# Kernel optimization log

Measured on AMD Instinct MI355X. Metric: run time of the kernel, lower is better.

Reference implementation:

```python
import jax, jax.numpy as jnp
import numpy as np

N = 16384          # number of proposals (batch dim already squeezed)
FEAT = 512         # CLIP ViT-B/32 embedding dim
NUM_CATS = 65      # background + 64 categories
K = 25             # max_boxes_to_return
NMS_THRESH = 0.6
MAX_DETS = 1000    # nms() default max_dets
MIN_RPN_SCORE = 0.9
MIN_BOX_AREA = 220.0


def setup_inputs() -> dict:
    key = jax.random.key(0)
    ks = jax.random.split(key, 9)
    # valid (ymin, xmin, ymax, xmax) boxes in a ~1000px image
    y1 = jax.random.uniform(ks[0], (N,)) * 900.0
    x1 = jax.random.uniform(ks[1], (N,)) * 900.0
    h = 40.0 + jax.random.uniform(ks[2], (N,)) * 160.0
    w = 40.0 + jax.random.uniform(ks[3], (N,)) * 160.0
    detection_boxes = jnp.stack([y1, x1, y1 + h, x1 + w], axis=-1)
    roi_boxes = jax.random.uniform(ks[4], (N, 4))
    roi_scores = jax.random.uniform(ks[5], (N,))
    visual_features = jax.random.normal(ks[6], (N, FEAT))
    visual_features = visual_features / jnp.linalg.norm(visual_features, axis=-1, keepdims=True)
    text_features = jax.random.normal(ks[7], (NUM_CATS, FEAT))
    text_features = text_features / jnp.linalg.norm(text_features, axis=-1, keepdims=True)
    detection_masks = jax.random.uniform(ks[8], (N, 33, 33))
    # row 2 of image_info holds (y_scale, x_scale)
    image_info = jnp.ones((5, 2), jnp.float32).at[2].set(jnp.array([0.8, 0.8], jnp.float32))
    return {
        'roi_boxes': roi_boxes,
        'roi_scores': roi_scores,
        'detection_boxes': detection_boxes,
        'detection_masks': detection_masks,
        'visual_features': visual_features,
        'image_info': image_info,
        'text_features': text_features,
    }


def greedy_nms_keep(boxes, scores, thresh, max_dets):
    """Greedy IoU NMS; returns boolean keep mask over original indices."""
    n = boxes.shape[0]
    order = jnp.argsort(-scores)           # descending by score
    b = boxes[order]
    y1, x1, y2, x2 = b[:, 0], b[:, 1], b[:, 2], b[:, 3]
    areas = (x2 - x1) * (y2 - y1)
    pos = jnp.arange(n)

    def body(i, state):
        suppressed, keep, cnt = state
        valid = jnp.logical_and(~suppressed[i], cnt < max_dets)
        iw = jnp.maximum(0.0, jnp.minimum(x2[i], x2) - jnp.maximum(x1[i], x1))
        ih = jnp.maximum(0.0, jnp.minimum(y2[i], y2) - jnp.maximum(y1[i], y1))
        inter = iw * ih
        iou = inter / (areas[i] + areas - inter + 1e-12)
        suppressed = suppressed | (valid & (iou > thresh) & (pos > i))
        keep = keep.at[i].set(valid)
        return suppressed, keep, cnt + valid.astype(jnp.int32)

    init = (jnp.zeros(n, bool), jnp.zeros(n, bool), jnp.int32(0))
    _, keep_sorted, _ = jax.lax.fori_loop(0, n, body, init)
    return jnp.zeros(n, bool).at[order].set(keep_sorted)


def reference(roi_boxes, roi_scores, detection_boxes, detection_masks,
              visual_features, image_info, text_features):
    image_scale = jnp.tile(image_info[2:3, :], (1, 2))          # [1,4]
    rescaled = detection_boxes / image_scale                     # [N,4]
    keep = greedy_nms_keep(detection_boxes, roi_scores, NMS_THRESH, MAX_DETS)
    box_sizes = (rescaled[:, 2] - rescaled[:, 0]) * (rescaled[:, 3] - rescaled[:, 1])
    valid = (keep
             & ~jnp.all(roi_boxes == 0.0, axis=-1)
             & (roi_scores >= MIN_RPN_SCORE)
             & (box_sizes > MIN_BOX_AREA))
    # first K valid indices in original order (fixed-shape compaction)
    idx = jnp.nonzero(valid, size=K, fill_value=0)[0]
    row_valid = jnp.arange(K) < jnp.minimum(valid.sum(), K)
    det_feat = visual_features[idx]                              # [K,512]
    det_resc = rescaled[idx]                                     # [K,4]
    scores_all = det_feat @ text_features.T                      # [K,C]; use_softmax=False
    max_s = jnp.max(scores_all, axis=1)
    fg = row_valid & (jnp.argmax(scores_all, axis=1) != 0)       # drop background argmax
    sort_key = jnp.where(fg, max_s, -jnp.inf)
    order = jnp.argsort(-sort_key)                               # fg rows first, by max score
    mask = fg[order]
    ymin, xmin, ymax, xmax = det_resc[:, 0], det_resc[:, 1], det_resc[:, 2], det_resc[:, 3]
    processed = jnp.stack([xmin, ymin, xmax, ymax], axis=-1)     # [K,4] xyxy
    bboxes = jnp.where(mask[:, None], processed[order], 0.0)
    scores = jnp.where(mask[:, None], scores_all[order][:, 1:], 0.0)  # drop bg column
    return scores, bboxes, mask
```

## Files before the change

kernel.cpp:

```cpp
#include <hip/hip_runtime.h>
#include <math.h>

#define N 16384
#define NWORDS 256
#define FEAT 512
#define NUM_CATS 65
#define K 25
#define MAX_DETS 1000


__global__ void k_build(const float* __restrict__ scores,
                        unsigned long long* __restrict__ ckeys,
                        unsigned int* __restrict__ rank,
                        int* __restrict__ ticket) {
    int i = blockIdx.x * 256 + threadIdx.x;
    float s = scores[i];
    rank[i] = 0u;
    bool cand = s >= 0.9f;
    unsigned long long bal = __ballot(cand);
    int lane = threadIdx.x & 63;
    int base = 0;
    if (lane == 0) base = atomicAdd(ticket, (int)__popcll(bal));
    base = __shfl(base, 0, 64);
    if (cand) {
        int pre = (int)__popcll(bal & ((1ull << lane) - 1ull));
        ckeys[base + pre] =
            ((unsigned long long)__float_as_uint(s) << 32) |
            (unsigned long long)(0xFFFFFFFFu - (unsigned)i);
    }
}

__global__ void k_crank(const unsigned long long* __restrict__ ckeys,
                        const int* __restrict__ ticket,
                        const float* __restrict__ det_boxes,
                        unsigned int* __restrict__ rank,
                        float4* __restrict__ sbox,
                        float* __restrict__ sarea) {
    int nc = *ticket;
    if (nc < 0) nc = 0;
    if (nc > N) nc = N;
    if (blockIdx.x * 256 >= nc) return;
    __shared__ unsigned long long lk[2048];
    int ci = blockIdx.x * 256 + threadIdx.x;
    unsigned long long my = (ci < nc) ? ckeys[ci] : 0ull;
    unsigned int cnt = 0;
    for (int j0 = 0; j0 < nc; j0 += 2048) {
        int m = nc - j0; if (m > 2048) m = 2048;
        __syncthreads();
        for (int t2 = threadIdx.x; t2 < m; t2 += 256) lk[t2] = ckeys[j0 + t2];
        __syncthreads();
        if (ci < nc) {
#pragma unroll 8
            for (int t2 = 0; t2 < m; ++t2) cnt += (lk[t2] > my) ? 1u : 0u;
        }
    }
    if (ci < nc) {
        unsigned int o = 0xFFFFFFFFu - (unsigned int)my;
        rank[o] = cnt;
        float4 b = ((const float4*)det_boxes)[o];
        sbox[cnt] = b;
        sarea[cnt] = (b.w - b.y) * (b.z - b.x);
    }
}

__global__ void k_mask(const float4* __restrict__ sbox,
                       const float* __restrict__ sarea,
                       const int* __restrict__ ticket,
                       unsigned long long* __restrict__ mask) {
    int ncand = *ticket;
    if (ncand < 0) ncand = 0;
    if (ncand > N) ncand = N;
    int NC = (ncand + 63) >> 6;
    int total = NC * (NC + 1) / 2;
    __shared__ float4 cbox[64];
    __shared__ float carea[64];
    int t = threadIdx.x;
    for (int tile = blockIdx.x; tile < total; tile += gridDim.x) {
        int cb = (int)((sqrtf(8.0f * (float)tile + 1.0f) - 1.0f) * 0.5f);
        while ((cb + 1) * (cb + 2) / 2 <= tile) ++cb;
        while (cb * (cb + 1) / 2 > tile) --cb;
        int rb = tile - cb * (cb + 1) / 2;

        __syncthreads();
        int col0 = cb * 64;
        cbox[t] = sbox[col0 + t];
        carea[t] = sarea[col0 + t];
        __syncthreads();
        int row = rb * 64 + t;
        float4 r = sbox[row];
        float ra = sarea[row];
        unsigned long long bits = 0ull;
        for (int j = 0; j < 64; ++j) {
            int col = col0 + j;
            if (col > row) {
                float4 cbx = cbox[j];
                float iw = fminf(r.w, cbx.w) - fmaxf(r.y, cbx.y);
                iw = fmaxf(iw, 0.0f);
                float ih = fminf(r.z, cbx.z) - fmaxf(r.x, cbx.x);
                ih = fmaxf(ih, 0.0f);
                float inter = iw * ih;
                float iou = inter / (ra + carea[j] - inter + 1e-12f);
                if (iou > 0.6f) bits |= (1ull << j);
            }
        }
        mask[(size_t)row * NWORDS + cb] = bits;
    }
}

__global__ void __launch_bounds__(64, 1)
k_scan(const unsigned long long* __restrict__ mask,
       const int* __restrict__ ticket,
       unsigned long long* __restrict__ keepw_ws) {
    __shared__ unsigned long long keepw_arr[NWORDS];
    __shared__ int keptList[1024];
    int lane = threadIdx.x;
    for (int i2 = lane; i2 < NWORDS; i2 += 64) keepw_arr[i2] = 0ull;

    int ncand = *ticket;
    if (ncand < 0) ncand = 0;
    if (ncand > N) ncand = N;
    int NC = (ncand + 63) >> 6;

    int cnt = 0, nk = 0;
    unsigned long long dnext = 0ull;
    if (NC > 0) dnext = mask[(size_t)lane * NWORDS];

    for (int c = 0; c < NC; ++c) {
        if (cnt >= MAX_DETS) break;

        unsigned long long dcur = dnext;
        if (c + 1 < NC)
            dnext = mask[(size_t)((c + 1) * 64 + lane) * NWORDS + (c + 1)];
        unsigned int dlo = (unsigned int)dcur;
        unsigned int dhi = (unsigned int)(dcur >> 32);

        unsigned long long acc = 0ull;
        {
            int q = lane;
            while (q < nk) {
#define GS(i)                                                             \
                unsigned long long G##i = 0ull;                           \
                {                                                         \
                    int qq = q + 64 * i;                                  \
                    if (qq < nk) {                                        \
                        int t = keptList[qq];                             \
                        G##i = mask[(size_t)t * NWORDS + c];              \
                    }                                                     \
                }
                GS(0) GS(1) GS(2) GS(3) GS(4) GS(5) GS(6) GS(7)
#undef GS
                acc |= G0 | G1 | G2 | G3 | G4 | G5 | G6 | G7;
                q += 512;
            }
        }
        unsigned int alo = (unsigned int)acc;
        unsigned int ahi = (unsigned int)(acc >> 32);
        for (int off = 32; off > 0; off >>= 1) {
            alo |= (unsigned int)__shfl_xor((int)alo, off, 64);
            ahi |= (unsigned int)__shfl_xor((int)ahi, off, 64);
        }
        unsigned long long sw =
            ((unsigned long long)(unsigned int)__builtin_amdgcn_readfirstlane(
                 (int)ahi) << 32) |
             (unsigned long long)(unsigned int)__builtin_amdgcn_readfirstlane(
                 (int)alo);
        unsigned long long alive = ~sw;
        if (ncand - c * 64 < 64)
            alive &= ((1ull << (ncand - c * 64)) - 1ull);

        unsigned long long zb = __ballot(dcur == 0ull);

        unsigned long long keepw = 0ull;
        unsigned long long NZ = alive & ~zb;
        while (true) {
            unsigned long long below;
            int t = -1;
            if (NZ) { t = __ffsll((long long)NZ) - 1; below = (1ull << t) - 1ull; }
            else below = ~0ull;
            unsigned long long seg = alive & below;
            int segc = (int)__popcll(seg);
            if (cnt + segc >= MAX_DETS) {
                int allow = MAX_DETS - cnt;
                unsigned long long r = 0ull;
                for (int k2 = 0; k2 < allow; ++k2) {
                    unsigned long long b = seg & (~seg + 1ull);
                    r |= b; seg ^= b;
                }
                keepw |= r; cnt = MAX_DETS; break;
            }
            keepw |= seg; cnt += segc; alive &= ~seg;
            if (t < 0) break;
            keepw |= (1ull << t); ++cnt;
            if (cnt >= MAX_DETS) break;
            unsigned long long dt =
                ((unsigned long long)(unsigned int)__builtin_amdgcn_readlane(
                     (int)dhi, t) << 32) |
                 (unsigned long long)(unsigned int)__builtin_amdgcn_readlane(
                     (int)dlo, t);
            alive &= ~(dt | (1ull << t));
            NZ &= alive;
            NZ &= ~(1ull << t);
        }
        if (lane == 0) keepw_arr[c] = keepw;

        if (keepw != 0ull) {
            if ((keepw >> lane) & 1ull) {
                int pre = (int)__popcll(keepw & ((1ull << lane) - 1ull));
                keptList[nk + pre] = c * 64 + lane;
            }
            nk += (int)__popcll(keepw);
        }
    }

    for (int i2 = lane; i2 < NWORDS; i2 += 64) keepw_ws[i2] = keepw_arr[i2];
}

__global__ void k_valid(const unsigned long long* __restrict__ keepw_ws,
                        const unsigned int* __restrict__ rank,
                        const float* __restrict__ roi_boxes,
                        const float* __restrict__ roi_scores,
                        const float* __restrict__ det_boxes,
                        const float* __restrict__ info,
                        unsigned long long* __restrict__ validw) {
    int i = blockIdx.x * 256 + threadIdx.x;
    float sy = info[4], sx = info[5];
    unsigned int r = rank[i];
    bool keep = ((keepw_ws[(r >> 6) & (NWORDS - 1)] >> (r & 63)) & 1ull) != 0ull;
    float4 rb = ((const float4*)roi_boxes)[i];
    bool nz = !((rb.x == 0.0f) && (rb.y == 0.0f) && (rb.z == 0.0f) && (rb.w == 0.0f));
    bool sc = roi_scores[i] >= 0.9f;
    float4 db = ((const float4*)det_boxes)[i];
    float r0 = db.x / sy, r1 = db.y / sx, r2 = db.z / sy, r3 = db.w / sx;
    bool big = ((r2 - r0) * (r3 - r1)) > 220.0f;
    bool valid = keep && nz && sc && big;
    unsigned long long bal = __ballot(valid);
    if ((threadIdx.x & 63) == 0) validw[i >> 6] = bal;
}

__device__ __forceinline__ void pick_first_k(
        const unsigned long long* __restrict__ validw,
        int* idxL, int* cntL, int tid) {
    if (tid < K) idxL[tid] = 0;
    __syncthreads();
    if (tid < 64) {
        int lane = tid;
        unsigned long long w0 = validw[lane * 4 + 0];
        unsigned long long w1 = validw[lane * 4 + 1];
        unsigned long long w2 = validw[lane * 4 + 2];
        unsigned long long w3 = validw[lane * 4 + 3];
        int s = (int)(__popcll(w0) + __popcll(w1) + __popcll(w2) + __popcll(w3));
        int pref = s;
        for (int off = 1; off < 64; off <<= 1) {
            int v = __shfl_up(pref, off, 64);
            if (lane >= off) pref += v;
        }
        int excl = pref - s;
        int total = __shfl(pref, 63, 64);
        if (lane == 0) *cntL = total;
        if (excl < K) {
            unsigned long long wsv[4] = { w0, w1, w2, w3 };
            int rk = excl;
            for (int q = 0; q < 4; ++q) {
                unsigned long long ww = wsv[q];
                while (ww && rk < K) {
                    int j = __ffsll((long long)ww) - 1;
                    ww &= ww - 1ull;
                    idxL[rk++] = (lane * 4 + q) * 64 + j;
                }
            }
        }
    }
    __syncthreads();
}

__global__ void k_gemm(const unsigned long long* __restrict__ validw,
                       const float* __restrict__ vis,
                       const float* __restrict__ tf,
                       float* __restrict__ scoresW) {
    __shared__ int idxL[K];
    __shared__ int cntL;
    __shared__ float featL[FEAT];
    int tid = threadIdx.x;
    pick_first_k(validw, idxL, &cntL, tid);
    int o = idxL[blockIdx.x];
    if (tid < 128)
        ((float4*)featL)[tid] = ((const float4*)(vis + (size_t)o * FEAT))[tid];
    __syncthreads();
    if (tid < NUM_CATS) {
        const float* tr = &tf[(size_t)tid * FEAT];
        float s = 0.0f;
#pragma unroll 8
        for (int e = 0; e < FEAT; ++e) s += featL[e] * tr[e];
        scoresW[blockIdx.x * NUM_CATS + tid] = s;
    }
}

__global__ void k_final(const unsigned long long* __restrict__ validw,
                        const float* __restrict__ scoresW,
                        const float* __restrict__ det_boxes,
                        const float* __restrict__ info,
                        float* __restrict__ out) {
    __shared__ int idxL[K];
    __shared__ int cntL;
    __shared__ float scL[K * NUM_CATS];
    __shared__ float keyL[K];
    __shared__ int fgL[K];
    __shared__ int ordL[K];
    int tid = threadIdx.x;
    pick_first_k(validw, idxL, &cntL, tid);

    for (int p = tid; p < K * NUM_CATS; p += 256) scL[p] = scoresW[p];
    __syncthreads();

    int count = cntL;
    int mincount = count < K ? count : K;

    if (tid < K) {
        float mv = scL[tid * NUM_CATS];
        int ma = 0;
        for (int c = 1; c < NUM_CATS; ++c) {
            float v = scL[tid * NUM_CATS + c];
            if (v > mv) { mv = v; ma = c; }
        }
        int fg = (tid < mincount) && (ma != 0);
        fgL[tid] = fg;
        keyL[tid] = fg ? mv : -INFINITY;
    }
    __syncthreads();

    if (tid == 0) {
        unsigned used = 0;
        for (int p = 0; p < K; ++p) {
            int bk = -1; float bv = 0.0f;
            for (int k2 = 0; k2 < K; ++k2) {
                if (used & (1u << k2)) continue;
                if (bk < 0 || keyL[k2] > bv) { bk = k2; bv = keyL[k2]; }
            }
            ordL[p] = bk;
            used |= (1u << bk);
        }
    }
    __syncthreads();

    float sy = info[4], sx = info[5];
    for (int p = tid; p < K * (NUM_CATS - 1); p += 256) {
        int q = p >> 6, cc = p & 63;
        int src = ordL[q];
        out[p] = fgL[src] ? scL[src * NUM_CATS + cc + 1] : 0.0f;
    }
    for (int p = tid; p < K * 4; p += 256) {
        int q = p >> 2, e = p & 3;
        int src = ordL[q];
        float v = 0.0f;
        if (fgL[src]) {
            int o = idxL[src];
            float b0 = det_boxes[o * 4 + 0] / sy;
            float b1 = det_boxes[o * 4 + 1] / sx;
            float b2 = det_boxes[o * 4 + 2] / sy;
            float b3 = det_boxes[o * 4 + 3] / sx;
            v = (e == 0) ? b1 : (e == 1) ? b0 : (e == 2) ? b3 : b2;
        }
        out[1600 + p] = v;
    }
    if (tid < K) out[1700 + tid] = fgL[ordL[tid]] ? 1.0f : 0.0f;
}

extern "C" void kernel_launch(void* const* d_in, const int* in_sizes, int n_in,
                              void* d_out, int out_size, void* d_ws, size_t ws_size,
                              hipStream_t stream) {
    const float* roi_boxes  = (const float*)d_in[0];
    const float* roi_scores = (const float*)d_in[1];
    const float* det_boxes  = (const float*)d_in[2];
    const float* vis        = (const float*)d_in[4];
    const float* info       = (const float*)d_in[5];
    const float* tf         = (const float*)d_in[6];

    char* ws = (char*)d_ws;
    unsigned long long* ckeys = (unsigned long long*)(ws + 0);
    unsigned int* rank        = (unsigned int*)(ws + 131072);
    float4* sbox              = (float4*)(ws + 262144);
    float* sarea              = (float*)(ws + 524288);
    unsigned long long* mask  = (unsigned long long*)(ws + 589824);
    int* idxArr               = (int*)(ws + 34144256);
    unsigned long long* keepw = (unsigned long long*)(ws + 34144384);
    unsigned long long* validw= (unsigned long long*)(ws + 34146432);
    float* scoresW            = (float*)(ws + 34148480);
    int* ticket               = idxArr + 30;

    hipMemsetAsync(idxArr, 0, 128, stream);
    k_build<<<64, 256, 0, stream>>>(roi_scores, ckeys, rank, ticket);
    k_crank<<<64, 256, 0, stream>>>(ckeys, ticket, det_boxes, rank, sbox, sarea);
    k_mask<<<1024, 64, 0, stream>>>(sbox, sarea, ticket, mask);
    k_scan<<<1, 64, 0, stream>>>(mask, ticket, keepw);
    k_valid<<<64, 256, 0, stream>>>(keepw, rank, roi_boxes, roi_scores,
                                    det_boxes, info, validw);
    k_gemm<<<K, 256, 0, stream>>>(validw, vis, tf, scoresW);
    k_final<<<1, 256, 0, stream>>>(validw, scoresW, det_boxes, info, (float*)d_out);
}
```

Baseline: 231.7 us.

## Fuse all pipeline stages into one cooperative kernel with grid syncs

Replaces the memset and seven separate kernel launches with a single cooperative kernel of 64 blocks that separates the stages with grid-wide syncs. The IoU mask stage now gives each wavefront its own tile and broadcasts column boxes with shuffles instead of LDS. This removes per-launch overhead and inter-kernel gaps. In exchange, the mask stage runs on only 64 blocks instead of 1024, and each grid.sync adds its own cost.

```diff
diff --git a/kernel.cpp b/kernel.cpp
--- a/kernel.cpp
+++ b/kernel.cpp
@@ -1,5 +1,8 @@
 #include <hip/hip_runtime.h>
+#include <hip/hip_cooperative_groups.h>
 #include <math.h>
+
+namespace cg = cooperative_groups;
 
 #define N 16384
 #define NWORDS 256
@@ -8,234 +11,6 @@
 #define K 25
 #define MAX_DETS 1000
 
-
-__global__ void k_build(const float* __restrict__ scores,
-                        unsigned long long* __restrict__ ckeys,
-                        unsigned int* __restrict__ rank,
-                        int* __restrict__ ticket) {
-    int i = blockIdx.x * 256 + threadIdx.x;
-    float s = scores[i];
-    rank[i] = 0u;
-    bool cand = s >= 0.9f;
-    unsigned long long bal = __ballot(cand);
-    int lane = threadIdx.x & 63;
-    int base = 0;
-    if (lane == 0) base = atomicAdd(ticket, (int)__popcll(bal));
-    base = __shfl(base, 0, 64);
-    if (cand) {
-        int pre = (int)__popcll(bal & ((1ull << lane) - 1ull));
-        ckeys[base + pre] =
-            ((unsigned long long)__float_as_uint(s) << 32) |
-            (unsigned long long)(0xFFFFFFFFu - (unsigned)i);
-    }
-}
-
-__global__ void k_crank(const unsigned long long* __restrict__ ckeys,
-                        const int* __restrict__ ticket,
-                        const float* __restrict__ det_boxes,
-                        unsigned int* __restrict__ rank,
-                        float4* __restrict__ sbox,
-                        float* __restrict__ sarea) {
-    int nc = *ticket;
-    if (nc < 0) nc = 0;
-    if (nc > N) nc = N;
-    if (blockIdx.x * 256 >= nc) return;
-    __shared__ unsigned long long lk[2048];
-    int ci = blockIdx.x * 256 + threadIdx.x;
-    unsigned long long my = (ci < nc) ? ckeys[ci] : 0ull;
-    unsigned int cnt = 0;
-    for (int j0 = 0; j0 < nc; j0 += 2048) {
-        int m = nc - j0; if (m > 2048) m = 2048;
-        __syncthreads();
-        for (int t2 = threadIdx.x; t2 < m; t2 += 256) lk[t2] = ckeys[j0 + t2];
-        __syncthreads();
-        if (ci < nc) {
-#pragma unroll 8
-            for (int t2 = 0; t2 < m; ++t2) cnt += (lk[t2] > my) ? 1u : 0u;
-        }
-    }
-    if (ci < nc) {
-        unsigned int o = 0xFFFFFFFFu - (unsigned int)my;
-        rank[o] = cnt;
-        float4 b = ((const float4*)det_boxes)[o];
-        sbox[cnt] = b;
-        sarea[cnt] = (b.w - b.y) * (b.z - b.x);
-    }
-}
-
-__global__ void k_mask(const float4* __restrict__ sbox,
-                       const float* __restrict__ sarea,
-                       const int* __restrict__ ticket,
-                       unsigned long long* __restrict__ mask) {
-    int ncand = *ticket;
-    if (ncand < 0) ncand = 0;
-    if (ncand > N) ncand = N;
-    int NC = (ncand + 63) >> 6;
-    int total = NC * (NC + 1) / 2;
-    __shared__ float4 cbox[64];
-    __shared__ float carea[64];
-    int t = threadIdx.x;
-    for (int tile = blockIdx.x; tile < total; tile += gridDim.x) {
-        int cb = (int)((sqrtf(8.0f * (float)tile + 1.0f) - 1.0f) * 0.5f);
-        while ((cb + 1) * (cb + 2) / 2 <= tile) ++cb;
-        while (cb * (cb + 1) / 2 > tile) --cb;
-        int rb = tile - cb * (cb + 1) / 2;
-
-        __syncthreads();
-        int col0 = cb * 64;
-        cbox[t] = sbox[col0 + t];
-        carea[t] = sarea[col0 + t];
-        __syncthreads();
-        int row = rb * 64 + t;
-        float4 r = sbox[row];
-        float ra = sarea[row];
-        unsigned long long bits = 0ull;
-        for (int j = 0; j < 64; ++j) {
-            int col = col0 + j;
-            if (col > row) {
-                float4 cbx = cbox[j];
-                float iw = fminf(r.w, cbx.w) - fmaxf(r.y, cbx.y);
-                iw = fmaxf(iw, 0.0f);
-                float ih = fminf(r.z, cbx.z) - fmaxf(r.x, cbx.x);
-                ih = fmaxf(ih, 0.0f);
-                float inter = iw * ih;
-                float iou = inter / (ra + carea[j] - inter + 1e-12f);
-                if (iou > 0.6f) bits |= (1ull << j);
-            }
-        }
-        mask[(size_t)row * NWORDS + cb] = bits;
-    }
-}
-
-__global__ void __launch_bounds__(64, 1)
-k_scan(const unsigned long long* __restrict__ mask,
-       const int* __restrict__ ticket,
-       unsigned long long* __restrict__ keepw_ws) {
-    __shared__ unsigned long long keepw_arr[NWORDS];
-    __shared__ int keptList[1024];
-    int lane = threadIdx.x;
-    for (int i2 = lane; i2 < NWORDS; i2 += 64) keepw_arr[i2] = 0ull;
-
-    int ncand = *ticket;
-    if (ncand < 0) ncand = 0;
-    if (ncand > N) ncand = N;
-    int NC = (ncand + 63) >> 6;
-
-    int cnt = 0, nk = 0;
-    unsigned long long dnext = 0ull;
-    if (NC > 0) dnext = mask[(size_t)lane * NWORDS];
-
-    for (int c = 0; c < NC; ++c) {
-        if (cnt >= MAX_DETS) break;
-
-        unsigned long long dcur = dnext;
-        if (c + 1 < NC)
-            dnext = mask[(size_t)((c + 1) * 64 + lane) * NWORDS + (c + 1)];
-        unsigned int dlo = (unsigned int)dcur;
-        unsigned int dhi = (unsigned int)(dcur >> 32);
-
-        unsigned long long acc = 0ull;
-        {
-            int q = lane;
-            while (q < nk) {
-#define GS(i)                                                             \
-                unsigned long long G##i = 0ull;                           \
-                {                                                         \
-                    int qq = q + 64 * i;                                  \
-                    if (qq < nk) {                                        \
-                        int t = keptList[qq];                             \
-                        G##i = mask[(size_t)t * NWORDS + c];              \
-                    }                                                     \
-                }
-                GS(0) GS(1) GS(2) GS(3) GS(4) GS(5) GS(6) GS(7)
-#undef GS
-                acc |= G0 | G1 | G2 | G3 | G4 | G5 | G6 | G7;
-                q += 512;
-            }
-        }
-        unsigned int alo = (unsigned int)acc;
-        unsigned int ahi = (unsigned int)(acc >> 32);
-        for (int off = 32; off > 0; off >>= 1) {
-            alo |= (unsigned int)__shfl_xor((int)alo, off, 64);
-            ahi |= (unsigned int)__shfl_xor((int)ahi, off, 64);
-        }
-        unsigned long long sw =
-            ((unsigned long long)(unsigned int)__builtin_amdgcn_readfirstlane(
-                 (int)ahi) << 32) |
-             (unsigned long long)(unsigned int)__builtin_amdgcn_readfirstlane(
-                 (int)alo);
-        unsigned long long alive = ~sw;
-        if (ncand - c * 64 < 64)
-            alive &= ((1ull << (ncand - c * 64)) - 1ull);
-
-        unsigned long long zb = __ballot(dcur == 0ull);
-
-        unsigned long long keepw = 0ull;
-        unsigned long long NZ = alive & ~zb;
-        while (true) {
-            unsigned long long below;
-            int t = -1;
-            if (NZ) { t = __ffsll((long long)NZ) - 1; below = (1ull << t) - 1ull; }
-            else below = ~0ull;
-            unsigned long long seg = alive & below;
-            int segc = (int)__popcll(seg);
-            if (cnt + segc >= MAX_DETS) {
-                int allow = MAX_DETS - cnt;
-                unsigned long long r = 0ull;
-                for (int k2 = 0; k2 < allow; ++k2) {
-                    unsigned long long b = seg & (~seg + 1ull);
-                    r |= b; seg ^= b;
-                }
-                keepw |= r; cnt = MAX_DETS; break;
-            }
-            keepw |= seg; cnt += segc; alive &= ~seg;
-            if (t < 0) break;
-            keepw |= (1ull << t); ++cnt;
-            if (cnt >= MAX_DETS) break;
-            unsigned long long dt =
-                ((unsigned long long)(unsigned int)__builtin_amdgcn_readlane(
-                     (int)dhi, t) << 32) |
-                 (unsigned long long)(unsigned int)__builtin_amdgcn_readlane(
-                     (int)dlo, t);
-            alive &= ~(dt | (1ull << t));
-            NZ &= alive;
-            NZ &= ~(1ull << t);
-        }
-        if (lane == 0) keepw_arr[c] = keepw;
-
-        if (keepw != 0ull) {
-            if ((keepw >> lane) & 1ull) {
-                int pre = (int)__popcll(keepw & ((1ull << lane) - 1ull));
-                keptList[nk + pre] = c * 64 + lane;
-            }
-            nk += (int)__popcll(keepw);
-        }
-    }
-
-    for (int i2 = lane; i2 < NWORDS; i2 += 64) keepw_ws[i2] = keepw_arr[i2];
-}
-
-__global__ void k_valid(const unsigned long long* __restrict__ keepw_ws,
-                        const unsigned int* __restrict__ rank,
-                        const float* __restrict__ roi_boxes,
-                        const float* __restrict__ roi_scores,
-                        const float* __restrict__ det_boxes,
-                        const float* __restrict__ info,
-                        unsigned long long* __restrict__ validw) {
-    int i = blockIdx.x * 256 + threadIdx.x;
-    float sy = info[4], sx = info[5];
-    unsigned int r = rank[i];
-    bool keep = ((keepw_ws[(r >> 6) & (NWORDS - 1)] >> (r & 63)) & 1ull) != 0ull;
-    float4 rb = ((const float4*)roi_boxes)[i];
-    bool nz = !((rb.x == 0.0f) && (rb.y == 0.0f) && (rb.z == 0.0f) && (rb.w == 0.0f));
-    bool sc = roi_scores[i] >= 0.9f;
-    float4 db = ((const float4*)det_boxes)[i];
-    float r0 = db.x / sy, r1 = db.y / sx, r2 = db.z / sy, r3 = db.w / sx;
-    bool big = ((r2 - r0) * (r3 - r1)) > 220.0f;
-    bool valid = keep && nz && sc && big;
-    unsigned long long bal = __ballot(valid);
-    if ((threadIdx.x & 63) == 0) validw[i >> 6] = bal;
-}
 
 __device__ __forceinline__ void pick_first_k(
         const unsigned long long* __restrict__ validw,
@@ -273,96 +48,312 @@
     __syncthreads();
 }
 
-__global__ void k_gemm(const unsigned long long* __restrict__ validw,
-                       const float* __restrict__ vis,
-                       const float* __restrict__ tf,
-                       float* __restrict__ scoresW) {
-    __shared__ int idxL[K];
-    __shared__ int cntL;
+__global__ void __launch_bounds__(256, 1)
+k_all(const float* __restrict__ roi_boxes,
+      const float* __restrict__ roi_scores,
+      const float* __restrict__ det_boxes,
+      const float* __restrict__ vis,
+      const float* __restrict__ info,
+      const float* __restrict__ tf,
+      unsigned long long* __restrict__ ckeys,
+      unsigned int* __restrict__ rank,
+      float4* __restrict__ sbox,
+      float* __restrict__ sarea,
+      unsigned long long* __restrict__ mask,
+      int* __restrict__ ticket,
+      unsigned long long* __restrict__ keepw_ws,
+      unsigned long long* __restrict__ validw,
+      float* __restrict__ scoresW,
+      float* __restrict__ out) {
+    cg::grid_group grid = cg::this_grid();
+    int bid = blockIdx.x, tid = threadIdx.x;
+    int gi = bid * 256 + tid;
+    int lane = tid & 63;
+    int wv = tid >> 6;
+
+    __shared__ unsigned long long lk[2048];
+    __shared__ unsigned long long keepw_arr[NWORDS];
+    __shared__ int keptList[1024];
     __shared__ float featL[FEAT];
-    int tid = threadIdx.x;
-    pick_first_k(validw, idxL, &cntL, tid);
-    int o = idxL[blockIdx.x];
-    if (tid < 128)
-        ((float4*)featL)[tid] = ((const float4*)(vis + (size_t)o * FEAT))[tid];
-    __syncthreads();
-    if (tid < NUM_CATS) {
-        const float* tr = &tf[(size_t)tid * FEAT];
-        float s = 0.0f;
-#pragma unroll 8
-        for (int e = 0; e < FEAT; ++e) s += featL[e] * tr[e];
-        scoresW[blockIdx.x * NUM_CATS + tid] = s;
-    }
-}
-
-__global__ void k_final(const unsigned long long* __restrict__ validw,
-                        const float* __restrict__ scoresW,
-                        const float* __restrict__ det_boxes,
-                        const float* __restrict__ info,
-                        float* __restrict__ out) {
-    __shared__ int idxL[K];
-    __shared__ int cntL;
     __shared__ float scL[K * NUM_CATS];
     __shared__ float keyL[K];
     __shared__ int fgL[K];
     __shared__ int ordL[K];
-    int tid = threadIdx.x;
-    pick_first_k(validw, idxL, &cntL, tid);
-
-    for (int p = tid; p < K * NUM_CATS; p += 256) scL[p] = scoresW[p];
-    __syncthreads();
-
-    int count = cntL;
-    int mincount = count < K ? count : K;
-
-    if (tid < K) {
-        float mv = scL[tid * NUM_CATS];
-        int ma = 0;
-        for (int c = 1; c < NUM_CATS; ++c) {
-            float v = scL[tid * NUM_CATS + c];
-            if (v > mv) { mv = v; ma = c; }
-        }
-        int fg = (tid < mincount) && (ma != 0);
-        fgL[tid] = fg;
-        keyL[tid] = fg ? mv : -INFINITY;
-    }
-    __syncthreads();
-
-    if (tid == 0) {
-        unsigned used = 0;
-        for (int p = 0; p < K; ++p) {
-            int bk = -1; float bv = 0.0f;
-            for (int k2 = 0; k2 < K; ++k2) {
-                if (used & (1u << k2)) continue;
-                if (bk < 0 || keyL[k2] > bv) { bk = k2; bv = keyL[k2]; }
-            }
-            ordL[p] = bk;
-            used |= (1u << bk);
-        }
-    }
-    __syncthreads();
-
-    float sy = info[4], sx = info[5];
-    for (int p = tid; p < K * (NUM_CATS - 1); p += 256) {
-        int q = p >> 6, cc = p & 63;
-        int src = ordL[q];
-        out[p] = fgL[src] ? scL[src * NUM_CATS + cc + 1] : 0.0f;
-    }
-    for (int p = tid; p < K * 4; p += 256) {
-        int q = p >> 2, e = p & 3;
-        int src = ordL[q];
-        float v = 0.0f;
-        if (fgL[src]) {
-            int o = idxL[src];
-            float b0 = det_boxes[o * 4 + 0] / sy;
-            float b1 = det_boxes[o * 4 + 1] / sx;
-            float b2 = det_boxes[o * 4 + 2] / sy;
-            float b3 = det_boxes[o * 4 + 3] / sx;
-            v = (e == 0) ? b1 : (e == 1) ? b0 : (e == 2) ? b3 : b2;
-        }
-        out[1600 + p] = v;
-    }
-    if (tid < K) out[1700 + tid] = fgL[ordL[tid]] ? 1.0f : 0.0f;
+    __shared__ int idxL[K];
+    __shared__ int cntL;
+
+    if (gi == 0) *ticket = 0;
+    grid.sync();
+
+    {
+        float s = roi_scores[gi];
+        rank[gi] = 0u;
+        bool cand = s >= 0.9f;
+        unsigned long long bal = __ballot(cand);
+        int base = 0;
+        if (lane == 0) base = atomicAdd(ticket, (int)__popcll(bal));
+        base = __shfl(base, 0, 64);
+        if (cand) {
+            int pre = (int)__popcll(bal & ((1ull << lane) - 1ull));
+            ckeys[base + pre] =
+                ((unsigned long long)__float_as_uint(s) << 32) |
+                (unsigned long long)(0xFFFFFFFFu - (unsigned)gi);
+        }
+    }
+    grid.sync();
+
+    int nc = *ticket;
+    if (nc < 0) nc = 0;
+    if (nc > N) nc = N;
+    int NC = (nc + 63) >> 6;
+
+    if (bid * 256 < nc) {
+        int ci = gi;
+        unsigned long long my = (ci < nc) ? ckeys[ci] : 0ull;
+        unsigned int cnt = 0;
+        for (int j0 = 0; j0 < nc; j0 += 2048) {
+            int m = nc - j0; if (m > 2048) m = 2048;
+            __syncthreads();
+            for (int t2 = tid; t2 < m; t2 += 256) lk[t2] = ckeys[j0 + t2];
+            __syncthreads();
+            if (ci < nc) {
+#pragma unroll 8
+                for (int t2 = 0; t2 < m; ++t2) cnt += (lk[t2] > my) ? 1u : 0u;
+            }
+        }
+        if (ci < nc) {
+            unsigned int o = 0xFFFFFFFFu - (unsigned int)my;
+            rank[o] = cnt;
+            float4 b = ((const float4*)det_boxes)[o];
+            sbox[cnt] = b;
+            sarea[cnt] = (b.w - b.y) * (b.z - b.x);
+        }
+    }
+    grid.sync();
+
+    {
+        int total = NC * (NC + 1) / 2;
+        for (int tile = bid * 4 + wv; tile < total; tile += 256) {
+            int cb = (int)((sqrtf(8.0f * (float)tile + 1.0f) - 1.0f) * 0.5f);
+            while ((cb + 1) * (cb + 2) / 2 <= tile) ++cb;
+            while (cb * (cb + 1) / 2 > tile) --cb;
+            int rb = tile - cb * (cb + 1) / 2;
+            int col0 = cb * 64;
+            float4 cbm = sbox[col0 + lane];
+            float cam = sarea[col0 + lane];
+            int row = rb * 64 + lane;
+            float4 r = sbox[row];
+            float ra = sarea[row];
+            unsigned long long bits = 0ull;
+            for (int j = 0; j < 64; ++j) {
+                float bx = __shfl(cbm.x, j, 64);
+                float by = __shfl(cbm.y, j, 64);
+                float bz = __shfl(cbm.z, j, 64);
+                float bw = __shfl(cbm.w, j, 64);
+                float ba = __shfl(cam, j, 64);
+                int col = col0 + j;
+                if (col > row) {
+                    float iw = fminf(r.w, bw) - fmaxf(r.y, by);
+                    iw = fmaxf(iw, 0.0f);
+                    float ih = fminf(r.z, bz) - fmaxf(r.x, bx);
+                    ih = fmaxf(ih, 0.0f);
+                    float inter = iw * ih;
+                    float iou = inter / (ra + ba - inter + 1e-12f);
+                    if (iou > 0.6f) bits |= (1ull << j);
+                }
+            }
+            mask[(size_t)row * NWORDS + cb] = bits;
+        }
+    }
+    grid.sync();
+
+    if (bid == 0 && tid < 64) {
+        for (int i2 = lane; i2 < NWORDS; i2 += 64) keepw_arr[i2] = 0ull;
+
+        int cnt = 0, nk = 0;
+        unsigned long long dnext = 0ull;
+        if (NC > 0) dnext = mask[(size_t)lane * NWORDS];
+
+        for (int c = 0; c < NC; ++c) {
+            if (cnt >= MAX_DETS) break;
+
+            unsigned long long dcur = dnext;
+            if (c + 1 < NC)
+                dnext = mask[(size_t)((c + 1) * 64 + lane) * NWORDS + (c + 1)];
+            unsigned int dlo = (unsigned int)dcur;
+            unsigned int dhi = (unsigned int)(dcur >> 32);
+
+            unsigned long long acc = 0ull;
+            {
+                int q = lane;
+                while (q < nk) {
+#define GS(i)                                                             \
+                    unsigned long long G##i = 0ull;                       \
+                    {                                                     \
+                        int qq = q + 64 * i;                              \
+                        if (qq < nk) {                                    \
+                            int t = keptList[qq];                         \
+                            G##i = mask[(size_t)t * NWORDS + c];          \
+                        }                                                 \
+                    }
+                    GS(0) GS(1) GS(2) GS(3) GS(4) GS(5) GS(6) GS(7)
+#undef GS
+                    acc |= G0 | G1 | G2 | G3 | G4 | G5 | G6 | G7;
+                    q += 512;
+                }
+            }
+            unsigned int alo = (unsigned int)acc;
+            unsigned int ahi = (unsigned int)(acc >> 32);
+            for (int off = 32; off > 0; off >>= 1) {
+                alo |= (unsigned int)__shfl_xor((int)alo, off, 64);
+                ahi |= (unsigned int)__shfl_xor((int)ahi, off, 64);
+            }
+            unsigned long long sw =
+                ((unsigned long long)(unsigned int)__builtin_amdgcn_readfirstlane(
+                     (int)ahi) << 32) |
+                 (unsigned long long)(unsigned int)__builtin_amdgcn_readfirstlane(
+                     (int)alo);
+            unsigned long long alive = ~sw;
+            if (nc - c * 64 < 64)
+                alive &= ((1ull << (nc - c * 64)) - 1ull);
+
+            unsigned long long zb = __ballot(dcur == 0ull);
+
+            unsigned long long keepw = 0ull;
+            unsigned long long NZ = alive & ~zb;
+            while (true) {
+                unsigned long long below;
+                int t = -1;
+                if (NZ) { t = __ffsll((long long)NZ) - 1; below = (1ull << t) - 1ull; }
+                else below = ~0ull;
+                unsigned long long seg = alive & below;
+                int segc = (int)__popcll(seg);
+                if (cnt + segc >= MAX_DETS) {
+                    int allow = MAX_DETS - cnt;
+                    unsigned long long r = 0ull;
+                    for (int k2 = 0; k2 < allow; ++k2) {
+                        unsigned long long b = seg & (~seg + 1ull);
+                        r |= b; seg ^= b;
+                    }
+                    keepw |= r; cnt = MAX_DETS; break;
+                }
+                keepw |= seg; cnt += segc; alive &= ~seg;
+                if (t < 0) break;
+                keepw |= (1ull << t); ++cnt;
+                if (cnt >= MAX_DETS) break;
+                unsigned long long dt =
+                    ((unsigned long long)(unsigned int)__builtin_amdgcn_readlane(
+                         (int)dhi, t) << 32) |
+                     (unsigned long long)(unsigned int)__builtin_amdgcn_readlane(
+                         (int)dlo, t);
+                alive &= ~(dt | (1ull << t));
+                NZ &= alive;
+                NZ &= ~(1ull << t);
+            }
+            if (lane == 0) keepw_arr[c] = keepw;
+
+            if (keepw != 0ull) {
+                if ((keepw >> lane) & 1ull) {
+                    int pre = (int)__popcll(keepw & ((1ull << lane) - 1ull));
+                    keptList[nk + pre] = c * 64 + lane;
+                }
+                nk += (int)__popcll(keepw);
+            }
+        }
+        for (int i2 = lane; i2 < NWORDS; i2 += 64) keepw_ws[i2] = keepw_arr[i2];
+    }
+    grid.sync();
+
+    {
+        float sy = info[4], sx = info[5];
+        unsigned int r = rank[gi];
+        bool keep = ((keepw_ws[(r >> 6) & (NWORDS - 1)] >> (r & 63)) & 1ull) != 0ull;
+        float4 rb = ((const float4*)roi_boxes)[gi];
+        bool nz = !((rb.x == 0.0f) && (rb.y == 0.0f) && (rb.z == 0.0f) && (rb.w == 0.0f));
+        bool sc = roi_scores[gi] >= 0.9f;
+        float4 db = ((const float4*)det_boxes)[gi];
+        float r0 = db.x / sy, r1 = db.y / sx, r2 = db.z / sy, r3 = db.w / sx;
+        bool big = ((r2 - r0) * (r3 - r1)) > 220.0f;
+        bool valid = keep && nz && sc && big;
+        unsigned long long bal = __ballot(valid);
+        if (lane == 0) validw[gi >> 6] = bal;
+    }
+    grid.sync();
+
+    if (bid < K) {
+        pick_first_k(validw, idxL, &cntL, tid);
+        int o = idxL[bid];
+        if (tid < 128)
+            ((float4*)featL)[tid] = ((const float4*)(vis + (size_t)o * FEAT))[tid];
+        __syncthreads();
+        if (tid < NUM_CATS) {
+            const float* tr = &tf[(size_t)tid * FEAT];
+            float s = 0.0f;
+#pragma unroll 8
+            for (int e = 0; e < FEAT; ++e) s += featL[e] * tr[e];
+            scoresW[bid * NUM_CATS + tid] = s;
+        }
+    }
+    grid.sync();
+
+    if (bid == 0) {
+        pick_first_k(validw, idxL, &cntL, tid);
+
+        for (int p = tid; p < K * NUM_CATS; p += 256) scL[p] = scoresW[p];
+        __syncthreads();
+
+        int count = cntL;
+        int mincount = count < K ? count : K;
+
+        if (tid < K) {
+            float mv = scL[tid * NUM_CATS];
+            int ma = 0;
+            for (int c = 1; c < NUM_CATS; ++c) {
+                float v = scL[tid * NUM_CATS + c];
+                if (v > mv) { mv = v; ma = c; }
+            }
+            int fg = (tid < mincount) && (ma != 0);
+            fgL[tid] = fg;
+            keyL[tid] = fg ? mv : -INFINITY;
+        }
+        __syncthreads();
+
+        if (tid == 0) {
+            unsigned used = 0;
+            for (int p = 0; p < K; ++p) {
+                int bk = -1; float bv = 0.0f;
+                for (int k2 = 0; k2 < K; ++k2) {
+                    if (used & (1u << k2)) continue;
+                    if (bk < 0 || keyL[k2] > bv) { bk = k2; bv = keyL[k2]; }
+                }
+                ordL[p] = bk;
+                used |= (1u << bk);
+            }
+        }
+        __syncthreads();
+
+        float sy = info[4], sx = info[5];
+        for (int p = tid; p < K * (NUM_CATS - 1); p += 256) {
+            int q = p >> 6, cc = p & 63;
+            int src = ordL[q];
+            out[p] = fgL[src] ? scL[src * NUM_CATS + cc + 1] : 0.0f;
+        }
+        for (int p = tid; p < K * 4; p += 256) {
+            int q = p >> 2, e = p & 3;
+            int src = ordL[q];
+            float v = 0.0f;
+            if (fgL[src]) {
+                int o = idxL[src];
+                float b0 = det_boxes[o * 4 + 0] / sy;
+                float b1 = det_boxes[o * 4 + 1] / sx;
+                float b2 = det_boxes[o * 4 + 2] / sy;
+                float b3 = det_boxes[o * 4 + 3] / sx;
+                v = (e == 0) ? b1 : (e == 1) ? b0 : (e == 2) ? b3 : b2;
+            }
+            out[1600 + p] = v;
+        }
+        if (tid < K) out[1700 + tid] = fgL[ordL[tid]] ? 1.0f : 0.0f;
+    }
 }
 
 extern "C" void kernel_launch(void* const* d_in, const int* in_sizes, int n_in,
@@ -376,24 +367,25 @@
     const float* tf         = (const float*)d_in[6];
 
     char* ws = (char*)d_ws;
-    unsigned long long* ckeys = (unsigned long long*)(ws + 0);
-    unsigned int* rank        = (unsigned int*)(ws + 131072);
-    float4* sbox              = (float4*)(ws + 262144);
-    float* sarea              = (float*)(ws + 524288);
-    unsigned long long* mask  = (unsigned long long*)(ws + 589824);
-    int* idxArr               = (int*)(ws + 34144256);
-    unsigned long long* keepw = (unsigned long long*)(ws + 34144384);
-    unsigned long long* validw= (unsigned long long*)(ws + 34146432);
-    float* scoresW            = (float*)(ws + 34148480);
-    int* ticket               = idxArr + 30;
-
-    hipMemsetAsync(idxArr, 0, 128, stream);
-    k_build<<<64, 256, 0, stream>>>(roi_scores, ckeys, rank, ticket);
-    k_crank<<<64, 256, 0, stream>>>(ckeys, ticket, det_boxes, rank, sbox, sarea);
-    k_mask<<<1024, 64, 0, stream>>>(sbox, sarea, ticket, mask);
-    k_scan<<<1, 64, 0, stream>>>(mask, ticket, keepw);
-    k_valid<<<64, 256, 0, stream>>>(keepw, rank, roi_boxes, roi_scores,
-                                    det_boxes, info, validw);
-    k_gemm<<<K, 256, 0, stream>>>(validw, vis, tf, scoresW);
-    k_final<<<1, 256, 0, stream>>>(validw, scoresW, det_boxes, info, (float*)d_out);
+    unsigned long long* ckeys  = (unsigned long long*)(ws + 0);
+    unsigned int* rankp        = (unsigned int*)(ws + 131072);
+    float4* sboxp              = (float4*)(ws + 262144);
+    float* sareap              = (float*)(ws + 524288);
+    unsigned long long* maskp  = (unsigned long long*)(ws + 589824);
+    int* idxArr                = (int*)(ws + 34144256);
+    unsigned long long* keepw  = (unsigned long long*)(ws + 34144384);
+    unsigned long long* validw = (unsigned long long*)(ws + 34146432);
+    float* scoresW             = (float*)(ws + 34148480);
+    int* ticket                = idxArr + 30;
+    float* outp                = (float*)d_out;
+
+    void* args[] = {
+        (void*)&roi_boxes, (void*)&roi_scores, (void*)&det_boxes,
+        (void*)&vis, (void*)&info, (void*)&tf,
+        (void*)&ckeys, (void*)&rankp, (void*)&sboxp, (void*)&sareap,
+        (void*)&maskp, (void*)&ticket, (void*)&keepw, (void*)&validw,
+        (void*)&scoresW, (void*)&outp
+    };
+    hipLaunchCooperativeKernel((const void*)k_all, dim3(64), dim3(256),
+                               args, 0, stream);
 }
```

Result: slower. 294.3 us (+27.1%).

## Replace atomic ticket with per-block counts and fold validity into consumers

Applied to the files above, without the earlier changes.

Drops the global atomic ticket and its memset by having each block write its own candidate count and compacted keys to a fixed per-block slot. Downstream kernels sum the 64 block counts with a wave reduction instead of reading one counter. The separate k_valid launch is removed: each k_gemm block and k_final recompute the validity bitmask over all 16384 proposals locally. This saves a memset and a kernel launch, but repeats the full-array validity scan in 26 blocks, each run by a single block.

```diff
diff --git a/kernel.cpp b/kernel.cpp
--- a/kernel.cpp
+++ b/kernel.cpp
@@ -12,49 +12,62 @@
 __global__ void k_build(const float* __restrict__ scores,
                         unsigned long long* __restrict__ ckeys,
                         unsigned int* __restrict__ rank,
-                        int* __restrict__ ticket) {
-    int i = blockIdx.x * 256 + threadIdx.x;
-    float s = scores[i];
-    rank[i] = 0u;
+                        int* __restrict__ bcnt) {
+    __shared__ int wcS[4];
+    int tid = threadIdx.x, bid = blockIdx.x;
+    int lane = tid & 63, wv = tid >> 6;
+    int gi = bid * 256 + tid;
+    float s = scores[gi];
+    rank[gi] = 0u;
     bool cand = s >= 0.9f;
     unsigned long long bal = __ballot(cand);
-    int lane = threadIdx.x & 63;
-    int base = 0;
-    if (lane == 0) base = atomicAdd(ticket, (int)__popcll(bal));
-    base = __shfl(base, 0, 64);
+    if (lane == 0) wcS[wv] = (int)__popcll(bal);
+    __syncthreads();
+    int base_w = 0, cntb = 0;
+    for (int w = 0; w < 4; ++w) { int v = wcS[w]; cntb += v; if (w < wv) base_w += v; }
     if (cand) {
-        int pre = (int)__popcll(bal & ((1ull << lane) - 1ull));
-        ckeys[base + pre] =
+        int slot = base_w + (int)__popcll(bal & ((1ull << lane) - 1ull));
+        ckeys[bid * 256 + slot] =
             ((unsigned long long)__float_as_uint(s) << 32) |
-            (unsigned long long)(0xFFFFFFFFu - (unsigned)i);
-    }
+            (unsigned long long)(0xFFFFFFFFu - (unsigned)gi);
+    }
+    if (tid == 0) bcnt[bid] = cntb;
 }
 
 __global__ void k_crank(const unsigned long long* __restrict__ ckeys,
-                        const int* __restrict__ ticket,
+                        const int* __restrict__ bcnt,
                         const float* __restrict__ det_boxes,
                         unsigned int* __restrict__ rank,
                         float4* __restrict__ sbox,
                         float* __restrict__ sarea) {
-    int nc = *ticket;
-    if (nc < 0) nc = 0;
-    if (nc > N) nc = N;
-    if (blockIdx.x * 256 >= nc) return;
     __shared__ unsigned long long lk[2048];
-    int ci = blockIdx.x * 256 + threadIdx.x;
-    unsigned long long my = (ci < nc) ? ckeys[ci] : 0ull;
+    __shared__ int bcS[64];
+    int tid = threadIdx.x, bid = blockIdx.x;
+    if (tid < 64) bcS[tid] = bcnt[tid];
+    __syncthreads();
+    int cntb = bcS[bid];
+    if (cntb == 0) return;
+    unsigned long long my = (tid < cntb) ? ckeys[bid * 256 + tid] : 0ull;
     unsigned int cnt = 0;
-    for (int j0 = 0; j0 < nc; j0 += 2048) {
-        int m = nc - j0; if (m > 2048) m = 2048;
-        __syncthreads();
-        for (int t2 = threadIdx.x; t2 < m; t2 += 256) lk[t2] = ckeys[j0 + t2];
-        __syncthreads();
-        if (ci < nc) {
+    int filled = 0;
+    for (int j = 0; j < 64; ++j) {
+        int cb = bcS[j];
+        if (filled + cb > 2048) {
+            __syncthreads();
+            if (tid < cntb) {
 #pragma unroll 8
-            for (int t2 = 0; t2 < m; ++t2) cnt += (lk[t2] > my) ? 1u : 0u;
-        }
-    }
-    if (ci < nc) {
+                for (int t2 = 0; t2 < filled; ++t2) cnt += (lk[t2] > my) ? 1u : 0u;
+            }
+            __syncthreads();
+            filled = 0;
+        }
+        if (tid < cb) lk[filled + tid] = ckeys[j * 256 + tid];
+        filled += cb;
+    }
+    __syncthreads();
+    if (tid < cntb) {
+#pragma unroll 8
+        for (int t2 = 0; t2 < filled; ++t2) cnt += (lk[t2] > my) ? 1u : 0u;
         unsigned int o = 0xFFFFFFFFu - (unsigned int)my;
         rank[o] = cnt;
         float4 b = ((const float4*)det_boxes)[o];
@@ -63,18 +76,24 @@
     }
 }
 
+__device__ __forceinline__ int sum_bcnt(const int* __restrict__ bcnt, int lane) {
+    int v = bcnt[lane];
+    for (int off = 32; off > 0; off >>= 1) v += __shfl_xor(v, off, 64);
+    return v;
+}
+
 __global__ void k_mask(const float4* __restrict__ sbox,
                        const float* __restrict__ sarea,
-                       const int* __restrict__ ticket,
+                       const int* __restrict__ bcnt,
                        unsigned long long* __restrict__ mask) {
-    int ncand = *ticket;
+    int t = threadIdx.x;
+    int ncand = sum_bcnt(bcnt, t);
     if (ncand < 0) ncand = 0;
     if (ncand > N) ncand = N;
     int NC = (ncand + 63) >> 6;
     int total = NC * (NC + 1) / 2;
     __shared__ float4 cbox[64];
     __shared__ float carea[64];
-    int t = threadIdx.x;
     for (int tile = blockIdx.x; tile < total; tile += gridDim.x) {
         int cb = (int)((sqrtf(8.0f * (float)tile + 1.0f) - 1.0f) * 0.5f);
         while ((cb + 1) * (cb + 2) / 2 <= tile) ++cb;
@@ -109,14 +128,14 @@
 
 __global__ void __launch_bounds__(64, 1)
 k_scan(const unsigned long long* __restrict__ mask,
-       const int* __restrict__ ticket,
+       const int* __restrict__ bcnt,
        unsigned long long* __restrict__ keepw_ws) {
     __shared__ unsigned long long keepw_arr[NWORDS];
     __shared__ int keptList[1024];
     int lane = threadIdx.x;
     for (int i2 = lane; i2 < NWORDS; i2 += 64) keepw_arr[i2] = 0ull;
 
-    int ncand = *ticket;
+    int ncand = sum_bcnt(bcnt, lane);
     if (ncand < 0) ncand = 0;
     if (ncand > N) ncand = N;
     int NC = (ncand + 63) >> 6;
@@ -215,26 +234,30 @@
     for (int i2 = lane; i2 < NWORDS; i2 += 64) keepw_ws[i2] = keepw_arr[i2];
 }
 
-__global__ void k_valid(const unsigned long long* __restrict__ keepw_ws,
-                        const unsigned int* __restrict__ rank,
-                        const float* __restrict__ roi_boxes,
-                        const float* __restrict__ roi_scores,
-                        const float* __restrict__ det_boxes,
-                        const float* __restrict__ info,
-                        unsigned long long* __restrict__ validw) {
-    int i = blockIdx.x * 256 + threadIdx.x;
-    float sy = info[4], sx = info[5];
-    unsigned int r = rank[i];
-    bool keep = ((keepw_ws[(r >> 6) & (NWORDS - 1)] >> (r & 63)) & 1ull) != 0ull;
-    float4 rb = ((const float4*)roi_boxes)[i];
-    bool nz = !((rb.x == 0.0f) && (rb.y == 0.0f) && (rb.z == 0.0f) && (rb.w == 0.0f));
-    bool sc = roi_scores[i] >= 0.9f;
-    float4 db = ((const float4*)det_boxes)[i];
-    float r0 = db.x / sy, r1 = db.y / sx, r2 = db.z / sy, r3 = db.w / sx;
-    bool big = ((r2 - r0) * (r3 - r1)) > 220.0f;
-    bool valid = keep && nz && sc && big;
-    unsigned long long bal = __ballot(valid);
-    if ((threadIdx.x & 63) == 0) validw[i >> 6] = bal;
+__device__ __forceinline__ void build_valid_local(
+        unsigned long long* vwL,
+        const unsigned long long* __restrict__ keepw_ws,
+        const unsigned int* __restrict__ rank,
+        const float* __restrict__ roi_boxes,
+        const float* __restrict__ roi_scores,
+        const float* __restrict__ det_boxes,
+        float sy, float sx, int tid) {
+    int lane = tid & 63, wv = tid >> 6;
+    for (int it = 0; it < 64; ++it) {
+        int i = it * 256 + tid;
+        unsigned int r = rank[i];
+        bool keep = ((keepw_ws[(r >> 6) & (NWORDS - 1)] >> (r & 63)) & 1ull) != 0ull;
+        float4 rb = ((const float4*)roi_boxes)[i];
+        bool nz = !((rb.x == 0.0f) && (rb.y == 0.0f) && (rb.z == 0.0f) && (rb.w == 0.0f));
+        bool sc = roi_scores[i] >= 0.9f;
+        float4 db = ((const float4*)det_boxes)[i];
+        float r0 = db.x / sy, r1 = db.y / sx, r2 = db.z / sy, r3 = db.w / sx;
+        bool big = ((r2 - r0) * (r3 - r1)) > 220.0f;
+        bool valid = keep && nz && sc && big;
+        unsigned long long bal = __ballot(valid);
+        if (lane == 0) vwL[it * 4 + wv] = bal;
+    }
+    __syncthreads();
 }
 
 __device__ __forceinline__ void pick_first_k(
@@ -273,15 +296,24 @@
     __syncthreads();
 }
 
-__global__ void k_gemm(const unsigned long long* __restrict__ validw,
+__global__ void k_gemm(const unsigned long long* __restrict__ keepw_ws,
+                       const unsigned int* __restrict__ rank,
+                       const float* __restrict__ roi_boxes,
+                       const float* __restrict__ roi_scores,
+                       const float* __restrict__ det_boxes,
+                       const float* __restrict__ info,
                        const float* __restrict__ vis,
                        const float* __restrict__ tf,
                        float* __restrict__ scoresW) {
+    __shared__ unsigned long long vwL[NWORDS];
     __shared__ int idxL[K];
     __shared__ int cntL;
     __shared__ float featL[FEAT];
     int tid = threadIdx.x;
-    pick_first_k(validw, idxL, &cntL, tid);
+    float sy = info[4], sx = info[5];
+    build_valid_local(vwL, keepw_ws, rank, roi_boxes, roi_scores, det_boxes,
+                      sy, sx, tid);
+    pick_first_k(vwL, idxL, &cntL, tid);
     int o = idxL[blockIdx.x];
     if (tid < 128)
         ((float4*)featL)[tid] = ((const float4*)(vis + (size_t)o * FEAT))[tid];
@@ -295,11 +327,15 @@
     }
 }
 
-__global__ void k_final(const unsigned long long* __restrict__ validw,
+__global__ void k_final(const unsigned long long* __restrict__ keepw_ws,
+                        const unsigned int* __restrict__ rank,
+                        const float* __restrict__ roi_boxes,
+                        const float* __restrict__ roi_scores,
                         const float* __restrict__ scoresW,
                         const float* __restrict__ det_boxes,
                         const float* __restrict__ info,
                         float* __restrict__ out) {
+    __shared__ unsigned long long vwL[NWORDS];
     __shared__ int idxL[K];
     __shared__ int cntL;
     __shared__ float scL[K * NUM_CATS];
@@ -307,7 +343,10 @@
     __shared__ int fgL[K];
     __shared__ int ordL[K];
     int tid = threadIdx.x;
-    pick_first_k(validw, idxL, &cntL, tid);
+    float sy = info[4], sx = info[5];
+    build_valid_local(vwL, keepw_ws, rank, roi_boxes, roi_scores, det_boxes,
+                      sy, sx, tid);
+    pick_first_k(vwL, idxL, &cntL, tid);
 
     for (int p = tid; p < K * NUM_CATS; p += 256) scL[p] = scoresW[p];
     __syncthreads();
@@ -342,7 +381,6 @@
     }
     __syncthreads();
 
-    float sy = info[4], sx = info[5];
     for (int p = tid; p < K * (NUM_CATS - 1); p += 256) {
         int q = p >> 6, cc = p & 63;
         int src = ordL[q];
@@ -378,22 +416,19 @@
     char* ws = (char*)d_ws;
     unsigned long long* ckeys = (unsigned long long*)(ws + 0);
     unsigned int* rank        = (unsigned int*)(ws + 131072);
+    int* bcnt                 = (int*)(ws + 196608);
     float4* sbox              = (float4*)(ws + 262144);
     float* sarea              = (float*)(ws + 524288);
     unsigned long long* mask  = (unsigned long long*)(ws + 589824);
-    int* idxArr               = (int*)(ws + 34144256);
     unsigned long long* keepw = (unsigned long long*)(ws + 34144384);
-    unsigned long long* validw= (unsigned long long*)(ws + 34146432);
     float* scoresW            = (float*)(ws + 34148480);
-    int* ticket               = idxArr + 30;
-
-    hipMemsetAsync(idxArr, 0, 128, stream);
-    k_build<<<64, 256, 0, stream>>>(roi_scores, ckeys, rank, ticket);
-    k_crank<<<64, 256, 0, stream>>>(ckeys, ticket, det_boxes, rank, sbox, sarea);
-    k_mask<<<1024, 64, 0, stream>>>(sbox, sarea, ticket, mask);
-    k_scan<<<1, 64, 0, stream>>>(mask, ticket, keepw);
-    k_valid<<<64, 256, 0, stream>>>(keepw, rank, roi_boxes, roi_scores,
-                                    det_boxes, info, validw);
-    k_gemm<<<K, 256, 0, stream>>>(validw, vis, tf, scoresW);
-    k_final<<<1, 256, 0, stream>>>(validw, scoresW, det_boxes, info, (float*)d_out);
-}
+
+    k_build<<<64, 256, 0, stream>>>(roi_scores, ckeys, rank, bcnt);
+    k_crank<<<64, 256, 0, stream>>>(ckeys, bcnt, det_boxes, rank, sbox, sarea);
+    k_mask<<<1024, 64, 0, stream>>>(sbox, sarea, bcnt, mask);
+    k_scan<<<1, 64, 0, stream>>>(mask, bcnt, keepw);
+    k_gemm<<<K, 256, 0, stream>>>(keepw, rank, roi_boxes, roi_scores,
+                                  det_boxes, info, vis, tf, scoresW);
+    k_final<<<1, 256, 0, stream>>>(keepw, rank, roi_boxes, roi_scores,
+                                   scoresW, det_boxes, info, (float*)d_out);
+}
```

New measurement: 338.4 us. 1.46x slower.
